# Kernel optimization log

Hardware: AMD Instinct MI355X
Metric: run time of the kernel (lower is better)

The kernel has to match this reference:

```python
import jax, jax.numpy as jnp
import numpy as np

D = 2048          # n_embd
H = 4 * D         # hidden_size
B, S = 4, 2048


def _make_masks(seed=0):
    rng = np.random.default_rng(seed)
    # mask1: for each group of 4 output rows, keep 2 of 4 rows (whole rows)
    mask1 = np.zeros((H, D), dtype=np.float32)
    for i in range(0, H, 4):
        keep = rng.permutation(4)[:2] + i
        mask1[keep, :] = 1.0
    # mask2: for each group of 4 input columns, keep 2 of 4 columns
    mask2 = np.zeros((D, H), dtype=np.float32)
    for i in range(0, H, 4):
        keep = rng.permutation(4)[:2] + i
        mask2[:, keep] = 1.0
    return jnp.asarray(mask1), jnp.asarray(mask2)


def setup_inputs() -> dict:
    key = jax.random.key(0)
    k_x, k_w1, k_w2 = jax.random.split(key, 3)
    x = jax.random.normal(k_x, (B, S, D), dtype=jnp.float32)
    # Kaiming-uniform-ish init like nn.Linear defaults
    w1 = jax.random.uniform(k_w1, (H, D), dtype=jnp.float32, minval=-1.0, maxval=1.0) / np.sqrt(D)
    w2 = jax.random.uniform(k_w2, (D, H), dtype=jnp.float32, minval=-1.0, maxval=1.0) / np.sqrt(H)
    mask1, mask2 = _make_masks()
    return {"x": x, "w1": w1, "w2": w2, "mask1": mask1, "mask2": mask2}


def reference(x, w1, w2, mask1, mask2):
    # sparse_multiply is elementwise mask application on the weights
    sw1 = w1 * mask1                      # [H, D]
    sw2 = w2 * mask2                      # [D, H]
    h = jnp.einsum('bsd,hd->bsh', x, sw1) # F.linear(x, sw1)
    h = jax.nn.gelu(h, approximate=False) # torch F.gelu default = exact erf
    out = jnp.einsum('bsh,dh->bsd', h, sw2)
    return out
```

## Files before the change

### kernel.cpp

```cpp
#include <hip/hip_runtime.h>
#include <hip/hip_bf16.h>

typedef __bf16 bf16_t;
typedef __bf16 bf16x8 __attribute__((ext_vector_type(8)));
typedef float f32x4 __attribute__((ext_vector_type(4)));

__device__ __forceinline__ unsigned short f32_to_bf16_rn(float f) {
  unsigned u = __float_as_uint(f);
  u += 0x7fffu + ((u >> 16) & 1u);
  return (unsigned short)(u >> 16);
}

__device__ __forceinline__ float gelu_exact(float x) {
  return 0.5f * x * (1.0f + erff(x * 0.7071067811865475f));
}

__global__ void cast_x_kernel(const float* __restrict__ in,
                              unsigned short* __restrict__ out, int n4) {
  int i = blockIdx.x * blockDim.x + threadIdx.x;
  if (i >= n4) return;
  float4 v = ((const float4*)in)[i];
  ushort4 o;
  o.x = f32_to_bf16_rn(v.x);
  o.y = f32_to_bf16_rn(v.y);
  o.z = f32_to_bf16_rn(v.z);
  o.w = f32_to_bf16_rn(v.w);
  ((ushort4*)out)[i] = o;
}

__global__ void build_idx_kernel(const float* __restrict__ mask1,
                                 const float* __restrict__ mask2,
                                 int* __restrict__ idx, int* __restrict__ meta,
                                 int H, int D) {
  __shared__ int sums[1024];
  const int t = threadIdx.x;
  int flags[8];
  int tot = 0;
#pragma unroll
  for (int u = 0; u < 8; ++u) {
    int j = t * 8 + u;
    int f = (mask1[(long long)j * D] != 0.0f) && (mask2[j] != 0.0f);
    flags[u] = f;
    tot += f;
  }
  sums[t] = tot;
  __syncthreads();
  for (int off = 1; off < 1024; off <<= 1) {
    int v = (t >= off) ? sums[t - off] : 0;
    __syncthreads();
    sums[t] += v;
    __syncthreads();
  }
  int pos = sums[t] - tot;
#pragma unroll
  for (int u = 0; u < 8; ++u) {
    if (flags[u]) idx[pos++] = t * 8 + u;
  }
  if (t == 1023) {
    int count = sums[1023];
    meta[0] = count;
    meta[1] = (count + 127) & ~127;
  }
}

__global__ void compact_w1_kernel(const float* __restrict__ w1,
                                  const int* __restrict__ idx,
                                  const int* __restrict__ meta,
                                  unsigned short* __restrict__ w1c, int D) {
  int q = blockIdx.x * blockDim.x + threadIdx.x;
  int k = q >> 9;
  int d4 = (q & 511) << 2;
  int count = meta[0];
  ushort4 o = {0, 0, 0, 0};
  if (k < count) {
    int j = idx[k];
    float4 v = *(const float4*)(w1 + (long long)j * D + d4);
    o.x = f32_to_bf16_rn(v.x);
    o.y = f32_to_bf16_rn(v.y);
    o.z = f32_to_bf16_rn(v.z);
    o.w = f32_to_bf16_rn(v.w);
  }
  *(ushort4*)(w1c + (long long)k * D + d4) = o;
}

__global__ void compact_w2_kernel(const float* __restrict__ w2,
                                  const int* __restrict__ idx,
                                  const int* __restrict__ meta,
                                  unsigned short* __restrict__ w2c, int H) {
  int q = blockIdx.x * blockDim.x + threadIdx.x;
  int n = q >> 10;
  int k4 = (q & 1023) << 2;
  int count = meta[0];
  ushort4 o = {0, 0, 0, 0};
  const float* src = w2 + (long long)n * H;
#pragma unroll
  for (int u = 0; u < 4; ++u) {
    int k = k4 + u;
    unsigned short v = 0;
    if (k < count) v = f32_to_bf16_rn(src[idx[k]]);
    ((unsigned short*)&o)[u] = v;
  }
  *(ushort4*)(w2c + (long long)n * 4096 + k4) = o;
}

#define BUF_STRIDE 65536
#define BREG_OFF 32768
#define HALF_STRIDE 16384
#define WAVE_STRIDE 2048
#define INST_STRIDE 1024

#define STAGE_A(c, h, i, k0)                                                   \
  __builtin_amdgcn_global_load_lds(                                            \
      (const __attribute__((address_space(1))) void*)(Asrc +                   \
          ((h) * 128 + (i) * 8) * ldA + (k0)),                                 \
      (__attribute__((address_space(3))) void*)(&smem[(c) * BUF_STRIDE +       \
          (h) * HALF_STRIDE + w * WAVE_STRIDE + (i) * INST_STRIDE]),           \
      16, 0, 0)

#define STAGE_B(c, h, i, k0)                                                   \
  __builtin_amdgcn_global_load_lds(                                            \
      (const __attribute__((address_space(1))) void*)(Bsrc +                   \
          ((h) * 128 + (i) * 8) * ldB + (k0)),                                 \
      (__attribute__((address_space(3))) void*)(&smem[(c) * BUF_STRIDE +       \
          BREG_OFF + (h) * HALF_STRIDE + w * WAVE_STRIDE + (i) * INST_STRIDE]),\
      16, 0, 0)

#define STAGE_TILE(c, k0)                                                      \
  do {                                                                         \
    STAGE_A(c, 0, 0, k0); STAGE_A(c, 0, 1, k0);                                \
    STAGE_A(c, 1, 0, k0); STAGE_A(c, 1, 1, k0);                                \
    STAGE_B(c, 0, 0, k0); STAGE_B(c, 0, 1, k0);                                \
    STAGE_B(c, 1, 0, k0); STAGE_B(c, 1, 1, k0);                                \
  } while (0)

template <int EPI>
__global__ __launch_bounds__(512, 2) void gemm256_kernel(
    const bf16_t* __restrict__ A, const bf16_t* __restrict__ B,
    void* __restrict__ Cout, long long ldA, long long ldB, long long ldC,
    int Kfix, const int* __restrict__ meta) {
  const int kpad = meta[1];
  const int nwg = gridDim.x * gridDim.y;
  const int bid = blockIdx.y * gridDim.x + blockIdx.x;
  const int swz = (bid & 7) * (nwg >> 3) + (bid >> 3);
  const int bx = swz % gridDim.x;
  const int by = swz / gridDim.x;
  const long long brow = (long long)by * 256;
  const long long bcol = (long long)bx * 256;
  if (EPI == 1 && bcol >= kpad) return;
  const int K = (EPI == 0) ? kpad : Kfix;
  const int NT = K >> 6;

  __shared__ __align__(16) char smem[131072];

  const int tid = threadIdx.x;
  const int l = tid & 63;
  const int w = tid >> 6;
  const int wm = w >> 2;
  const int wn = w & 3;

  const int srow = w * 16 + (l >> 3);
  const int sgran = (l & 7) ^ (l >> 3);
  const bf16_t* Asrc = A + (brow + srow) * ldA + sgran * 8;
  const bf16_t* Bsrc = B + (bcol + srow) * ldB + sgran * 8;

  const int g0 = (l >> 4) ^ (l & 7);
  const int aoff = (wm * 128 + (l & 15)) * 128 + g0 * 16;
  const int boff = BREG_OFF + (wn * 64 + (l & 15)) * 128 + g0 * 16;

  f32x4 acc[8][4];
#pragma unroll
  for (int m = 0; m < 8; ++m)
#pragma unroll
    for (int n = 0; n < 4; ++n) acc[m][n] = (f32x4){0.f, 0.f, 0.f, 0.f};

  bf16x8 a[8][2], b[4][2];

  STAGE_TILE(0, 0);
  __syncthreads();

  for (int t = 0; t < NT; ++t) {
    const int c = t & 1;
    const int cb = c * BUF_STRIDE;
    if (t + 1 < NT) {
      const int k1 = (t + 1) << 6;
      STAGE_TILE(c ^ 1, k1);
    }
#pragma unroll
    for (int m = 0; m < 8; ++m)
#pragma unroll
      for (int kk = 0; kk < 2; ++kk)
        a[m][kk] = *(const bf16x8*)&smem[cb + ((aoff + m * 2048) ^ (kk * 64))];
#pragma unroll
    for (int n = 0; n < 4; ++n)
#pragma unroll
      for (int kk = 0; kk < 2; ++kk)
        b[n][kk] = *(const bf16x8*)&smem[cb + ((boff + n * 2048) ^ (kk * 64))];
#pragma unroll
    for (int kk = 0; kk < 2; ++kk)
#pragma unroll
      for (int m = 0; m < 8; ++m)
#pragma unroll
        for (int n = 0; n < 4; ++n)
          acc[m][n] = __builtin_amdgcn_mfma_f32_16x16x32_bf16(
              a[m][kk], b[n][kk], acc[m][n], 0, 0, 0);
    __syncthreads();
  }

  const int orow = wm * 128 + ((l >> 4) << 2);
  const int ocol = wn * 64 + (l & 15);
#pragma unroll
  for (int m = 0; m < 8; ++m)
#pragma unroll
    for (int n = 0; n < 4; ++n)
#pragma unroll
      for (int r = 0; r < 4; ++r) {
        long long row = brow + orow + m * 16 + r;
        long long col = bcol + ocol + n * 16;
        float v = acc[m][n][r];
        if (EPI == 1) {
          ((unsigned short*)Cout)[row * ldC + col] =
              f32_to_bf16_rn(gelu_exact(v));
        } else {
          ((float*)Cout)[row * ldC + col] = v;
        }
      }
}

extern "C" void kernel_launch(void* const* d_in, const int* in_sizes, int n_in,
                              void* d_out, int out_size, void* d_ws,
                              size_t ws_size, hipStream_t stream) {
  const float* x = (const float*)d_in[0];
  const float* w1 = (const float*)d_in[1];
  const float* w2 = (const float*)d_in[2];
  const float* mask1 = (const float*)d_in[3];
  const float* mask2 = (const float*)d_in[4];
  float* out = (float*)d_out;

  const int D = 2048, H = 8192, M = 8192;
  const int KP = 4096;

  char* ws = (char*)d_ws;
  unsigned short* xb = (unsigned short*)ws;
  unsigned short* w1c = xb + (size_t)M * D;
  unsigned short* w2c = w1c + (size_t)KP * D;
  unsigned short* hb = w2c + (size_t)D * KP;
  int* idx = (int*)(hb + (size_t)M * KP);
  int* meta = idx + KP;

  build_idx_kernel<<<1, 1024, 0, stream>>>(mask1, mask2, idx, meta, H, D);

  {
    int n4 = (M * D) / 4;
    cast_x_kernel<<<n4 / 256, 256, 0, stream>>>(x, xb, n4);
  }
  {
    int nq = KP * (D / 4);
    compact_w1_kernel<<<nq / 256, 256, 0, stream>>>(w1, idx, meta, w1c, D);
  }
  {
    int nq = D * (KP / 4);
    compact_w2_kernel<<<nq / 256, 256, 0, stream>>>(w2, idx, meta, w2c, H);
  }

  {
    dim3 grid(KP / 256, M / 256);
    gemm256_kernel<1><<<grid, 512, 0, stream>>>(
        (const bf16_t*)xb, (const bf16_t*)w1c, hb, (long long)D, (long long)D,
        (long long)KP, D, meta);
  }
  {
    dim3 grid(D / 256, M / 256);
    gemm256_kernel<0><<<grid, 512, 0, stream>>>(
        (const bf16_t*)hb, (const bf16_t*)w2c, out, (long long)KP,
        (long long)KP, (long long)D, 0, meta);
  }
}
```

Baseline: 271.0 us.

## Shrink GEMM tiles to 256x128 with K=32 steps and 256-thread blocks

```diff
diff --git a/kernel.cpp b/kernel.cpp
--- a/kernel.cpp
+++ b/kernel.cpp
@@ -103,38 +103,34 @@
   *(ushort4*)(w2c + (long long)n * 4096 + k4) = o;
 }
 
-#define BUF_STRIDE 65536
-#define BREG_OFF 32768
-#define HALF_STRIDE 16384
-#define WAVE_STRIDE 2048
-#define INST_STRIDE 1024
-
-#define STAGE_A(c, h, i, k0)                                                   \
+#define TBUF 24576
+#define BOFF 16384
+
+#define STAGE_A(c, jj, k0)                                                     \
   __builtin_amdgcn_global_load_lds(                                            \
-      (const __attribute__((address_space(1))) void*)(Asrc +                   \
-          ((h) * 128 + (i) * 8) * ldA + (k0)),                                 \
-      (__attribute__((address_space(3))) void*)(&smem[(c) * BUF_STRIDE +       \
-          (h) * HALF_STRIDE + w * WAVE_STRIDE + (i) * INST_STRIDE]),           \
+      (const __attribute__((address_space(1))) void*)(AsrcB +                  \
+          (long long)(jj) * 16 * ldA + (k0)),                                  \
+      (__attribute__((address_space(3))) void*)(&smem[(c) * TBUF +             \
+          (w * 4 + (jj)) * 1024]),                                             \
       16, 0, 0)
 
-#define STAGE_B(c, h, i, k0)                                                   \
+#define STAGE_B(c, jj, k0)                                                     \
   __builtin_amdgcn_global_load_lds(                                            \
-      (const __attribute__((address_space(1))) void*)(Bsrc +                   \
-          ((h) * 128 + (i) * 8) * ldB + (k0)),                                 \
-      (__attribute__((address_space(3))) void*)(&smem[(c) * BUF_STRIDE +       \
-          BREG_OFF + (h) * HALF_STRIDE + w * WAVE_STRIDE + (i) * INST_STRIDE]),\
+      (const __attribute__((address_space(1))) void*)(BsrcB +                  \
+          (long long)(jj) * 16 * ldB + (k0)),                                  \
+      (__attribute__((address_space(3))) void*)(&smem[(c) * TBUF + BOFF +      \
+          (w * 2 + (jj)) * 1024]),                                             \
       16, 0, 0)
 
 #define STAGE_TILE(c, k0)                                                      \
   do {                                                                         \
-    STAGE_A(c, 0, 0, k0); STAGE_A(c, 0, 1, k0);                                \
-    STAGE_A(c, 1, 0, k0); STAGE_A(c, 1, 1, k0);                                \
-    STAGE_B(c, 0, 0, k0); STAGE_B(c, 0, 1, k0);                                \
-    STAGE_B(c, 1, 0, k0); STAGE_B(c, 1, 1, k0);                                \
+    STAGE_A(c, 0, k0); STAGE_A(c, 1, k0);                                      \
+    STAGE_A(c, 2, k0); STAGE_A(c, 3, k0);                                      \
+    STAGE_B(c, 0, k0); STAGE_B(c, 1, k0);                                      \
   } while (0)
 
 template <int EPI>
-__global__ __launch_bounds__(512, 2) void gemm256_kernel(
+__global__ __launch_bounds__(256, 2) void gemm256x128_kernel(
     const bf16_t* __restrict__ A, const bf16_t* __restrict__ B,
     void* __restrict__ Cout, long long ldA, long long ldB, long long ldC,
     int Kfix, const int* __restrict__ meta) {
@@ -145,27 +141,25 @@
   const int bx = swz % gridDim.x;
   const int by = swz / gridDim.x;
   const long long brow = (long long)by * 256;
-  const long long bcol = (long long)bx * 256;
+  const long long bcol = (long long)bx * 128;
   if (EPI == 1 && bcol >= kpad) return;
   const int K = (EPI == 0) ? kpad : Kfix;
-  const int NT = K >> 6;
-
-  __shared__ __align__(16) char smem[131072];
+  const int NT = K >> 5;
+
+  __shared__ __align__(16) char smem[2 * TBUF];
 
   const int tid = threadIdx.x;
   const int l = tid & 63;
   const int w = tid >> 6;
-  const int wm = w >> 2;
-  const int wn = w & 3;
-
-  const int srow = w * 16 + (l >> 3);
-  const int sgran = (l & 7) ^ (l >> 3);
-  const bf16_t* Asrc = A + (brow + srow) * ldA + sgran * 8;
-  const bf16_t* Bsrc = B + (bcol + srow) * ldB + sgran * 8;
-
-  const int g0 = (l >> 4) ^ (l & 7);
-  const int aoff = (wm * 128 + (l & 15)) * 128 + g0 * 16;
-  const int boff = BREG_OFF + (wn * 64 + (l & 15)) * 128 + g0 * 16;
+  const int wm = w >> 1;
+  const int wn = w & 1;
+
+  const int srow4 = l >> 2;
+  const int sg = ((l & 3) ^ ((l >> 3) & 3)) * 8;
+  const bf16_t* AsrcB = A + (brow + w * 64 + srow4) * ldA + sg;
+  const bf16_t* BsrcB = B + (bcol + w * 32 + srow4) * ldB + sg;
+
+  const int g0a = (((l >> 4) ^ ((l >> 1) & 3)) * 16);
 
   f32x4 acc[8][4];
 #pragma unroll
@@ -173,36 +167,32 @@
 #pragma unroll
     for (int n = 0; n < 4; ++n) acc[m][n] = (f32x4){0.f, 0.f, 0.f, 0.f};
 
-  bf16x8 a[8][2], b[4][2];
+  bf16x8 a[8], b[4];
 
   STAGE_TILE(0, 0);
   __syncthreads();
 
   for (int t = 0; t < NT; ++t) {
     const int c = t & 1;
-    const int cb = c * BUF_STRIDE;
+    const int cb = c * TBUF;
     if (t + 1 < NT) {
-      const int k1 = (t + 1) << 6;
+      const int k1 = (t + 1) << 5;
       STAGE_TILE(c ^ 1, k1);
     }
 #pragma unroll
     for (int m = 0; m < 8; ++m)
-#pragma unroll
-      for (int kk = 0; kk < 2; ++kk)
-        a[m][kk] = *(const bf16x8*)&smem[cb + ((aoff + m * 2048) ^ (kk * 64))];
+      a[m] = *(const bf16x8*)&smem[cb + (wm * 128 + m * 16 + (l & 15)) * 64 +
+                                   g0a];
 #pragma unroll
     for (int n = 0; n < 4; ++n)
-#pragma unroll
-      for (int kk = 0; kk < 2; ++kk)
-        b[n][kk] = *(const bf16x8*)&smem[cb + ((boff + n * 2048) ^ (kk * 64))];
-#pragma unroll
-    for (int kk = 0; kk < 2; ++kk)
-#pragma unroll
-      for (int m = 0; m < 8; ++m)
-#pragma unroll
-        for (int n = 0; n < 4; ++n)
-          acc[m][n] = __builtin_amdgcn_mfma_f32_16x16x32_bf16(
-              a[m][kk], b[n][kk], acc[m][n], 0, 0, 0);
+      b[n] = *(const bf16x8*)&smem[cb + BOFF +
+                                   (wn * 64 + n * 16 + (l & 15)) * 64 + g0a];
+#pragma unroll
+    for (int m = 0; m < 8; ++m)
+#pragma unroll
+      for (int n = 0; n < 4; ++n)
+        acc[m][n] = __builtin_amdgcn_mfma_f32_16x16x32_bf16(a[m], b[n],
+                                                            acc[m][n], 0, 0, 0);
     __syncthreads();
   }
 
@@ -263,14 +253,14 @@
   }
 
   {
-    dim3 grid(KP / 256, M / 256);
-    gemm256_kernel<1><<<grid, 512, 0, stream>>>(
+    dim3 grid(KP / 128, M / 256);
+    gemm256x128_kernel<1><<<grid, 256, 0, stream>>>(
         (const bf16_t*)xb, (const bf16_t*)w1c, hb, (long long)D, (long long)D,
         (long long)KP, D, meta);
   }
   {
-    dim3 grid(D / 256, M / 256);
-    gemm256_kernel<0><<<grid, 512, 0, stream>>>(
+    dim3 grid(D / 128, M / 256);
+    gemm256x128_kernel<0><<<grid, 256, 0, stream>>>(
         (const bf16_t*)hb, (const bf16_t*)w2c, out, (long long)KP,
         (long long)KP, (long long)D, 0, meta);
   }
```

Result: slower. 286.5 us (+5.7%).
